# Optimization experiments

Measured on AMD Instinct MI355X. Metric: run time of the kernel, lower is better.

The kernel has to match this reference:

```python
import jax, jax.numpy as jnp
import numpy as np

B = 16384  # batch
D = 1024   # input_size (== hidden_size, required by the original code)
H = 1024   # hidden_size


def setup_inputs() -> dict:
    key = jax.random.key(0)
    ks = jax.random.split(key, 20)
    s = 0.02
    inp = {
        "x": jax.random.normal(ks[0], (B, D), dtype=jnp.float32),
        "h": jax.random.normal(ks[1], (B, H), dtype=jnp.float32),
        "c_prev": jax.random.normal(ks[2], (B, H), dtype=jnp.float32),
    }
    names = ["i_x", "f_x", "c_x", "o_x", "i_h", "f_h", "c_h", "o_h"]
    for n, name in enumerate(names):
        in_dim = D if name.endswith("_x") else H
        inp["W" + name] = jax.random.normal(ks[3 + 2 * n], (H, in_dim), dtype=jnp.float32) * s
        inp["b" + name] = jax.random.normal(ks[4 + 2 * n], (H,), dtype=jnp.float32) * s
    return inp


def reference(x, h, c_prev,
              Wi_x, bi_x, Wf_x, bf_x, Wc_x, bc_x, Wo_x, bo_x,
              Wi_h, bi_h, Wf_h, bf_h, Wc_h, bc_h, Wo_h, bo_h):
    # NOTE: the original module applies NO sigmoid to the gates; i, f, o are raw affine sums.
    i = x @ Wi_x.T + bi_x + h @ Wi_h.T + bi_h
    f = x @ Wf_x.T + bf_x + h @ Wf_h.T + bf_h
    g = jnp.tanh(x @ Wc_x.T + bc_x + h @ Wc_h.T + bc_h)
    o = x @ Wo_x.T + bo_x + h @ Wo_h.T + bo_h
    c_next = g * i + c_prev * f
    h_next = o * jnp.tanh(c_next)
    return (h_next, c_next)
```

## Files before the change

### kernel.cpp

```cpp
#include <hip/hip_runtime.h>
#include <hip/hip_bf16.h>


#define MROWS 16384
#define NCOLS 1024
#define KTOT  2048

typedef __attribute__((ext_vector_type(8))) short bf16x8;
typedef __attribute__((ext_vector_type(4))) float f32x4;
typedef unsigned int u32;
typedef unsigned short u16;

__device__ __forceinline__ u16 f2bf(float f) {
  union { float f; u32 u; } v; v.f = f;
  u32 r = v.u + 0x7fffu + ((v.u >> 16) & 1u);
  return (u16)(r >> 16);
}

__device__ __forceinline__ bf16x8 pack8(float4 lo, float4 hi) {
  bf16x8 v;
  v[0] = (short)f2bf(lo.x); v[1] = (short)f2bf(lo.y);
  v[2] = (short)f2bf(lo.z); v[3] = (short)f2bf(lo.w);
  v[4] = (short)f2bf(hi.x); v[5] = (short)f2bf(hi.y);
  v[6] = (short)f2bf(hi.z); v[7] = (short)f2bf(hi.w);
  return v;
}

__device__ __forceinline__ float tanh_fast(float x) {
  float e = __expf(2.0f * x);
  return 1.0f - 2.0f / (e + 1.0f);
}

typedef __attribute__((address_space(1))) const u32 gas_u32;
typedef __attribute__((address_space(3))) u32 las_u32;

__device__ __forceinline__ void gl_lds16(const void* g, void* l) {
  __builtin_amdgcn_global_load_lds((gas_u32*)g, (las_u32*)l, 16, 0, 0);
}

__global__ void __launch_bounds__(256) convA(const float* __restrict__ x,
                                             const float* __restrict__ h,
                                             u16* __restrict__ A) {
  u32 t = blockIdx.x * 256u + threadIdx.x;
  #pragma unroll
  for (int i = 0; i < 4; ++i) {
    u32 chunk = t + (u32)i * 1048576u;
    u32 row = chunk >> 8;
    u32 cpos = (chunk & 255u) * 8u;
    const float* src = (cpos < 1024u) ? (x + (size_t)row * 1024 + cpos)
                                      : (h + (size_t)row * 1024 + (cpos - 1024u));
    float4 lo = *(const float4*)src;
    float4 hi = *(const float4*)(src + 4);
    *(bf16x8*)(A + (size_t)chunk * 8) = pack8(lo, hi);
  }
}

__global__ void __launch_bounds__(256) convW(const float* __restrict__ wix, const float* __restrict__ wfx,
                                             const float* __restrict__ wcx, const float* __restrict__ wox,
                                             const float* __restrict__ wih, const float* __restrict__ wfh,
                                             const float* __restrict__ wch, const float* __restrict__ woh,
                                             u16* __restrict__ W) {
  u32 t = blockIdx.x * 256u + threadIdx.x;
  const float* WX[4] = {wix, wfx, wcx, wox};
  const float* WH[4] = {wih, wfh, wch, woh};
  #pragma unroll
  for (int g = 0; g < 4; ++g) {
    u32 c3 = t;
    u32 n = c3 >> 8;
    u32 cpos = (c3 & 255u) * 8u;
    const float* src = (cpos < 1024u) ? (WX[g] + (size_t)n * 1024 + cpos)
                                      : (WH[g] + (size_t)n * 1024 + (cpos - 1024u));
    float4 lo = *(const float4*)src;
    float4 hi = *(const float4*)(src + 4);
    *(bf16x8*)(W + (size_t)g * 2097152 + (size_t)c3 * 8) = pack8(lo, hi);
  }
}

template <bool FAST>
__global__ void __launch_bounds__(256, 2) lstm_gemm(
    const u16* __restrict__ Abf, const u16* __restrict__ Wbf,
    const float* __restrict__ x, const float* __restrict__ h,
    const float* __restrict__ wix, const float* __restrict__ wfx,
    const float* __restrict__ wcx, const float* __restrict__ wox,
    const float* __restrict__ wih, const float* __restrict__ wfh,
    const float* __restrict__ wch, const float* __restrict__ woh,
    const float* __restrict__ bix, const float* __restrict__ bfx,
    const float* __restrict__ bcx, const float* __restrict__ box_,
    const float* __restrict__ bih, const float* __restrict__ bfh,
    const float* __restrict__ bch, const float* __restrict__ boh,
    const float* __restrict__ cprev, float* __restrict__ out) {
  __shared__ alignas(16) u16 sA[128 * 64];
  __shared__ alignas(16) u16 sB[4 * 64 * 64];

  const u32 tid = threadIdx.x;
  const u32 lane = tid & 63u;
  const u32 wid = tid >> 6;
  const u32 wr = wid >> 1, wc = wid & 1u;
  const u32 bidx = blockIdx.x;
  const u32 bm = bidx >> 4, bn = bidx & 15u;

  f32x4 acc[4][4][2];
  #pragma unroll
  for (int g = 0; g < 4; ++g)
    #pragma unroll
    for (int m = 0; m < 4; ++m)
      #pragma unroll
      for (int n = 0; n < 2; ++n)
        acc[g][m][n] = (f32x4){0.f, 0.f, 0.f, 0.f};

  const u32 l15 = lane & 15u, l4 = lane >> 4;

  for (int kt = 0; kt < KTOT / 64; ++kt) {
    const u32 k0 = (u32)kt * 64u;
    if (kt) __syncthreads();

    if constexpr (FAST) {
      #pragma unroll
      for (int j = 0; j < 4; ++j) {
        u32 chunk = (wid * 4u + j) * 64u + lane;
        u32 row = chunk >> 3;
        u32 cole = ((chunk & 7u) * 8u) ^ ((row & 7u) << 3);
        const u16* g = Abf + (size_t)(bm * 128u + row) * KTOT + k0 + cole;
        gl_lds16((const void*)g, (void*)(sA + (wid * 4u + j) * 512u));
      }
      #pragma unroll
      for (int j = 0; j < 8; ++j) {
        u32 chunk = (wid * 8u + j) * 64u + lane;
        u32 gate = chunk >> 9;
        u32 c3 = chunk & 511u;
        u32 row = c3 >> 3;
        u32 cole = ((c3 & 7u) * 8u) ^ ((row & 7u) << 3);
        const u16* g = Wbf + (size_t)gate * 2097152 + (size_t)(bn * 64u + row) * KTOT + k0 + cole;
        gl_lds16((const void*)g, (void*)(sB + (wid * 8u + j) * 512u));
      }
    } else {
      #pragma unroll
      for (int c = 0; c < 4; ++c) {
        u32 chunk = tid + (u32)c * 256u;
        u32 row = chunk >> 3;
        u32 cp = (chunk & 7u) * 8u;
        u32 gk = k0 + cp;
        const float* src = (gk < 1024u) ? (x + (size_t)(bm * 128u + row) * 1024 + gk)
                                        : (h + (size_t)(bm * 128u + row) * 1024 + (gk - 1024u));
        float4 lo = *(const float4*)src;
        float4 hi = *(const float4*)(src + 4);
        u32 dst = row * 128u + ((cp * 2u) ^ ((row & 7u) << 4));
        *(bf16x8*)((char*)sA + dst) = pack8(lo, hi);
      }
      #pragma unroll
      for (int g = 0; g < 4; ++g) {
        const float* Wxg = (g == 0) ? wix : (g == 1) ? wfx : (g == 2) ? wcx : wox;
        const float* Whg = (g == 0) ? wih : (g == 1) ? wfh : (g == 2) ? wch : woh;
        #pragma unroll
        for (int cc = 0; cc < 2; ++cc) {
          u32 c3 = tid + (u32)cc * 256u;
          u32 row = c3 >> 3;
          u32 cp = (c3 & 7u) * 8u;
          u32 gk = k0 + cp;
          const float* src = (gk < 1024u) ? (Wxg + (size_t)(bn * 64u + row) * 1024 + gk)
                                          : (Whg + (size_t)(bn * 64u + row) * 1024 + (gk - 1024u));
          float4 lo = *(const float4*)src;
          float4 hi = *(const float4*)(src + 4);
          u32 dst = (u32)g * 8192u + row * 128u + ((cp * 2u) ^ ((row & 7u) << 4));
          *(bf16x8*)((char*)sB + dst) = pack8(lo, hi);
        }
      }
    }
    __syncthreads();

    #pragma unroll
    for (int s = 0; s < 2; ++s) {
      bf16x8 af[4];
      #pragma unroll
      for (int m = 0; m < 4; ++m) {
        u32 mrow = wr * 64u + (u32)m * 16u + l15;
        u32 off = mrow * 128u + (((u32)s * 64u + l4 * 16u) ^ ((mrow & 7u) << 4));
        af[m] = *(const bf16x8*)((const char*)sA + off);
      }
      #pragma unroll
      for (int g = 0; g < 4; ++g) {
        #pragma unroll
        for (int nf = 0; nf < 2; ++nf) {
          u32 nrow = wc * 32u + (u32)nf * 16u + l15;
          u32 off = (u32)g * 8192u + nrow * 128u +
                    (((u32)s * 64u + l4 * 16u) ^ ((nrow & 7u) << 4));
          bf16x8 bfr = *(const bf16x8*)((const char*)sB + off);
          #pragma unroll
          for (int m = 0; m < 4; ++m)
            acc[g][m][nf] = __builtin_amdgcn_mfma_f32_16x16x32_bf16(af[m], bfr, acc[g][m][nf], 0, 0, 0);
        }
      }
    }
  }

  #pragma unroll
  for (int nf = 0; nf < 2; ++nf) {
    u32 col = bn * 64u + wc * 32u + (u32)nf * 16u + l15;
    float bi = bix[col] + bih[col];
    float bff = bfx[col] + bfh[col];
    float bc = bcx[col] + bch[col];
    float bo = box_[col] + boh[col];
    #pragma unroll
    for (int m = 0; m < 4; ++m) {
      u32 row0 = bm * 128u + wr * 64u + (u32)m * 16u + l4 * 4u;
      #pragma unroll
      for (int r = 0; r < 4; ++r) {
        size_t idx = (size_t)(row0 + (u32)r) * 1024 + col;
        float iv = acc[0][m][nf][r] + bi;
        float fv = acc[1][m][nf][r] + bff;
        float gv = tanh_fast(acc[2][m][nf][r] + bc);
        float ov = acc[3][m][nf][r] + bo;
        float cp = cprev[idx];
        float cn = gv * iv + cp * fv;
        out[idx] = ov * tanh_fast(cn);
        out[(size_t)16777216 + idx] = cn;
      }
    }
  }
}

extern "C" void kernel_launch(void* const* d_in, const int* in_sizes, int n_in,
                              void* d_out, int out_size, void* d_ws, size_t ws_size,
                              hipStream_t stream) {
  const float* x = (const float*)d_in[0];
  const float* h = (const float*)d_in[1];
  const float* cprev = (const float*)d_in[2];
  const float* wix = (const float*)d_in[3];  const float* bix = (const float*)d_in[4];
  const float* wfx = (const float*)d_in[5];  const float* bfx = (const float*)d_in[6];
  const float* wcx = (const float*)d_in[7];  const float* bcx = (const float*)d_in[8];
  const float* wox = (const float*)d_in[9];  const float* box_ = (const float*)d_in[10];
  const float* wih = (const float*)d_in[11]; const float* bih = (const float*)d_in[12];
  const float* wfh = (const float*)d_in[13]; const float* bfh = (const float*)d_in[14];
  const float* wch = (const float*)d_in[15]; const float* bch = (const float*)d_in[16];
  const float* woh = (const float*)d_in[17]; const float* boh = (const float*)d_in[18];
  float* out = (float*)d_out;

  const size_t needA = (size_t)MROWS * KTOT * 2;
  const size_t needW = (size_t)4 * NCOLS * KTOT * 2;

  if (ws_size >= needA + needW) {
    u16* Abf = (u16*)d_ws;
    u16* Wbf = (u16*)((char*)d_ws + needA);
    convA<<<dim3(4096), dim3(256), 0, stream>>>(x, h, Abf);
    convW<<<dim3(1024), dim3(256), 0, stream>>>(wix, wfx, wcx, wox, wih, wfh, wch, woh, Wbf);
    lstm_gemm<true><<<dim3(2048), dim3(256), 0, stream>>>(
        Abf, Wbf, nullptr, nullptr,
        nullptr, nullptr, nullptr, nullptr, nullptr, nullptr, nullptr, nullptr,
        bix, bfx, bcx, box_, bih, bfh, bch, boh, cprev, out);
  } else {
    lstm_gemm<false><<<dim3(2048), dim3(256), 0, stream>>>(
        nullptr, nullptr, x, h,
        wix, wfx, wcx, wox, wih, wfh, wch, woh,
        bix, bfx, bcx, box_, bih, bfh, bch, boh, cprev, out);
  }
}
```

Measured before the change: 319.2 us.

## Replace fast-path GEMM with 256x256-tile, 8-wave, double-buffered ping-pong kernel

Introduces a new fast-path kernel that uses 512-thread blocks computing 256-row by 64-column (times 4 gates) output tiles. It double-buffers LDS with async global-to-LDS loads issued one or two k-tiles ahead, and splits each k-step into four MFMA phases separated by barriers, with raised wave priority around the MFMA blocks. Blocks are remapped with a grid swizzle for L2 locality, and the gates are interleaved so each wave holds all four gates for the same columns. The aim is to raise arithmetic intensity and hide load latency. In exchange it adds heavy barrier synchronisation and register pressure, and occupancy may fall to one block per CU.

Result: slower. 342.3 us (+7.2%).

```diff
diff --git a/kernel.cpp b/kernel.cpp
--- a/kernel.cpp
+++ b/kernel.cpp
@@ -76,9 +76,205 @@
   }
 }
 
-template <bool FAST>
-__global__ void __launch_bounds__(256, 2) lstm_gemm(
+#define SBAR() __builtin_amdgcn_sched_barrier(0)
+
+__global__ void __launch_bounds__(512) lstm_gemm8(
     const u16* __restrict__ Abf, const u16* __restrict__ Wbf,
+    const float* __restrict__ bix, const float* __restrict__ bfx,
+    const float* __restrict__ bcx, const float* __restrict__ box_,
+    const float* __restrict__ bih, const float* __restrict__ bfh,
+    const float* __restrict__ bch, const float* __restrict__ boh,
+    const float* __restrict__ cprev, float* __restrict__ out) {
+  __shared__ alignas(16) u16 sA[2 * 16384];
+  __shared__ alignas(16) u16 sB[2 * 16384];
+
+  const u32 tid = threadIdx.x;
+  const u32 lane = tid & 63u, wid = tid >> 6;
+  const u32 wr = wid >> 2, wc = wid & 3u;
+  const u32 l15 = lane & 15u, l4 = lane >> 4;
+
+  const u32 bid = blockIdx.x;
+  const u32 sid = (bid & 7u) * 128u + (bid >> 3);
+  const u32 bm = sid >> 4, bn = sid & 15u;
+
+  const u16* gA[2][2];
+  const u16* gB[2][2];
+  #pragma unroll
+  for (int h = 0; h < 2; ++h)
+    #pragma unroll
+    for (int j = 0; j < 2; ++j) {
+      u32 chunk = (wid * 2u + (u32)j) * 64u + lane;
+      u32 row = chunk >> 3, c = chunk & 7u;
+      u32 col16 = c ^ (row & 7u);
+      gA[h][j] = Abf + (size_t)(bm * 256u + (u32)h * 128u + row) * KTOT + col16 * 8u;
+      u32 fr = (u32)h * 128u + row;
+      u32 fi = fr >> 4;
+      u32 Wrow = (fi & 3u) * 1024u + bn * 64u + (fi >> 2) * 16u + (fr & 15u);
+      gB[h][j] = Wbf + (size_t)Wrow * KTOT + col16 * 8u;
+    }
+
+#define STAGE_A(ktile, dbuf) do { \
+    gl_lds16(gA[0][0] + (ktile) * 64, sA + (dbuf) * 16384u + (wid * 2u + 0u) * 512u); \
+    gl_lds16(gA[0][1] + (ktile) * 64, sA + (dbuf) * 16384u + (wid * 2u + 1u) * 512u); \
+    gl_lds16(gA[1][0] + (ktile) * 64, sA + (dbuf) * 16384u + 8192u + (wid * 2u + 0u) * 512u); \
+    gl_lds16(gA[1][1] + (ktile) * 64, sA + (dbuf) * 16384u + 8192u + (wid * 2u + 1u) * 512u); } while (0)
+#define STAGE_B_H(ktile, dbuf, hh) do { \
+    gl_lds16(gB[hh][0] + (ktile) * 64, sB + (dbuf) * 16384u + (hh) * 8192u + (wid * 2u + 0u) * 512u); \
+    gl_lds16(gB[hh][1] + (ktile) * 64, sB + (dbuf) * 16384u + (hh) * 8192u + (wid * 2u + 1u) * 512u); } while (0)
+
+  const char* cA = (const char*)sA;
+  const char* cB = (const char*)sB;
+  const u32 swzk[2] = { ((0u * 4u + l4) ^ (l15 & 7u)) << 4, ((1u * 4u + l4) ^ (l15 & 7u)) << 4 };
+
+  f32x4 acc[8][4];
+  #pragma unroll
+  for (int mf = 0; mf < 8; ++mf)
+    #pragma unroll
+    for (int gf = 0; gf < 4; ++gf)
+      acc[mf][gf] = (f32x4){0.f, 0.f, 0.f, 0.f};
+
+  STAGE_A(0, 0);
+  STAGE_B_H(0, 0, 0); STAGE_B_H(0, 0, 1);
+  STAGE_A(1, 1);
+  SBAR();
+  asm volatile("s_waitcnt vmcnt(4)" ::: "memory");
+  __builtin_amdgcn_s_barrier();
+  SBAR();
+
+  #pragma unroll 2
+  for (int kt = 0; kt < 32; ++kt) {
+    const u32 d = (u32)kt & 1u, dn = d ^ 1u;
+    const u32 dA = d * 32768u, dB = d * 32768u;
+    bf16x8 a03[4][2], a47[4][2], b01[2][2], b23[2][2];
+
+    #pragma unroll
+    for (int mf = 0; mf < 4; ++mf) {
+      u32 rb = dA + (wr * 128u + (u32)mf * 16u + l15) * 128u;
+      a03[mf][0] = *(const bf16x8*)(cA + rb + swzk[0]);
+      a03[mf][1] = *(const bf16x8*)(cA + rb + swzk[1]);
+    }
+    #pragma unroll
+    for (int gf = 0; gf < 2; ++gf) {
+      u32 rb = dB + (wc * 64u + (u32)gf * 16u + l15) * 128u;
+      b01[gf][0] = *(const bf16x8*)(cB + rb + swzk[0]);
+      b01[gf][1] = *(const bf16x8*)(cB + rb + swzk[1]);
+    }
+    if (kt < 31) STAGE_B_H(kt + 1, dn, 0);
+    SBAR();
+    __builtin_amdgcn_s_barrier();
+    asm volatile("s_waitcnt lgkmcnt(0)" ::: "memory");
+    SBAR();
+    __builtin_amdgcn_s_setprio(1);
+    #pragma unroll
+    for (int ks = 0; ks < 2; ++ks)
+      #pragma unroll
+      for (int gf = 0; gf < 2; ++gf)
+        #pragma unroll
+        for (int mf = 0; mf < 4; ++mf)
+          acc[mf][gf] = __builtin_amdgcn_mfma_f32_16x16x32_bf16(a03[mf][ks], b01[gf][ks], acc[mf][gf], 0, 0, 0);
+    __builtin_amdgcn_s_setprio(0);
+    SBAR();
+    __builtin_amdgcn_s_barrier();
+    SBAR();
+
+    #pragma unroll
+    for (int gf = 0; gf < 2; ++gf) {
+      u32 rb = dB + (wc * 64u + (2u + (u32)gf) * 16u + l15) * 128u;
+      b23[gf][0] = *(const bf16x8*)(cB + rb + swzk[0]);
+      b23[gf][1] = *(const bf16x8*)(cB + rb + swzk[1]);
+    }
+    if (kt < 31) STAGE_B_H(kt + 1, dn, 1);
+    SBAR();
+    __builtin_amdgcn_s_barrier();
+    asm volatile("s_waitcnt lgkmcnt(0)" ::: "memory");
+    SBAR();
+    __builtin_amdgcn_s_setprio(1);
+    #pragma unroll
+    for (int ks = 0; ks < 2; ++ks)
+      #pragma unroll
+      for (int gf = 0; gf < 2; ++gf)
+        #pragma unroll
+        for (int mf = 0; mf < 4; ++mf)
+          acc[mf][2 + gf] = __builtin_amdgcn_mfma_f32_16x16x32_bf16(a03[mf][ks], b23[gf][ks], acc[mf][2 + gf], 0, 0, 0);
+    __builtin_amdgcn_s_setprio(0);
+    SBAR();
+    __builtin_amdgcn_s_barrier();
+    SBAR();
+
+    #pragma unroll
+    for (int mf = 0; mf < 4; ++mf) {
+      u32 rb = dA + (wr * 128u + (4u + (u32)mf) * 16u + l15) * 128u;
+      a47[mf][0] = *(const bf16x8*)(cA + rb + swzk[0]);
+      a47[mf][1] = *(const bf16x8*)(cA + rb + swzk[1]);
+    }
+    SBAR();
+    __builtin_amdgcn_s_barrier();
+    asm volatile("s_waitcnt lgkmcnt(0)" ::: "memory");
+    SBAR();
+    __builtin_amdgcn_s_setprio(1);
+    #pragma unroll
+    for (int ks = 0; ks < 2; ++ks)
+      #pragma unroll
+      for (int gf = 0; gf < 2; ++gf)
+        #pragma unroll
+        for (int mf = 0; mf < 4; ++mf)
+          acc[4 + mf][gf] = __builtin_amdgcn_mfma_f32_16x16x32_bf16(a47[mf][ks], b01[gf][ks], acc[4 + mf][gf], 0, 0, 0);
+    __builtin_amdgcn_s_setprio(0);
+    SBAR();
+    __builtin_amdgcn_s_barrier();
+    SBAR();
+
+    if (kt < 30) {
+      STAGE_A(kt + 2, d);
+      SBAR();
+      asm volatile("s_waitcnt vmcnt(4)" ::: "memory");
+    } else if (kt == 30) {
+      SBAR();
+      asm volatile("s_waitcnt vmcnt(0)" ::: "memory");
+    }
+    SBAR();
+    __builtin_amdgcn_s_barrier();
+    SBAR();
+    __builtin_amdgcn_s_setprio(1);
+    #pragma unroll
+    for (int ks = 0; ks < 2; ++ks)
+      #pragma unroll
+      for (int gf = 0; gf < 2; ++gf)
+        #pragma unroll
+        for (int mf = 0; mf < 4; ++mf)
+          acc[4 + mf][2 + gf] = __builtin_amdgcn_mfma_f32_16x16x32_bf16(a47[mf][ks], b23[gf][ks], acc[4 + mf][2 + gf], 0, 0, 0);
+    __builtin_amdgcn_s_setprio(0);
+    SBAR();
+    __builtin_amdgcn_s_barrier();
+    SBAR();
+  }
+
+  const u32 col = bn * 64u + wc * 16u + l15;
+  const float bi = bix[col] + bih[col];
+  const float bff = bfx[col] + bfh[col];
+  const float bc = bcx[col] + bch[col];
+  const float bo = box_[col] + boh[col];
+  #pragma unroll
+  for (int mf = 0; mf < 8; ++mf) {
+    u32 row0 = bm * 256u + wr * 128u + (u32)mf * 16u + l4 * 4u;
+    #pragma unroll
+    for (int r = 0; r < 4; ++r) {
+      size_t idx = (size_t)(row0 + (u32)r) * 1024 + col;
+      float iv = acc[mf][0][r] + bi;
+      float fv = acc[mf][1][r] + bff;
+      float gv = tanh_fast(acc[mf][2][r] + bc);
+      float ov = acc[mf][3][r] + bo;
+      float cp = cprev[idx];
+      float cn = gv * iv + cp * fv;
+      out[idx] = ov * tanh_fast(cn);
+      out[(size_t)16777216 + idx] = cn;
+    }
+  }
+#undef STAGE_A
+#undef STAGE_B_H
+}
+
+__global__ void __launch_bounds__(256, 2) lstm_gemm_fb(
     const float* __restrict__ x, const float* __restrict__ h,
     const float* __restrict__ wix, const float* __restrict__ wfx,
     const float* __restrict__ wcx, const float* __restrict__ wox,
@@ -91,14 +287,12 @@
     const float* __restrict__ cprev, float* __restrict__ out) {
   __shared__ alignas(16) u16 sA[128 * 64];
   __shared__ alignas(16) u16 sB[4 * 64 * 64];
-
   const u32 tid = threadIdx.x;
   const u32 lane = tid & 63u;
   const u32 wid = tid >> 6;
   const u32 wr = wid >> 1, wc = wid & 1u;
   const u32 bidx = blockIdx.x;
   const u32 bm = bidx >> 4, bn = bidx & 15u;
-
   f32x4 acc[4][4][2];
   #pragma unroll
   for (int g = 0; g < 4; ++g)
@@ -107,67 +301,42 @@
       #pragma unroll
       for (int n = 0; n < 2; ++n)
         acc[g][m][n] = (f32x4){0.f, 0.f, 0.f, 0.f};
-
   const u32 l15 = lane & 15u, l4 = lane >> 4;
-
   for (int kt = 0; kt < KTOT / 64; ++kt) {
     const u32 k0 = (u32)kt * 64u;
     if (kt) __syncthreads();
-
-    if constexpr (FAST) {
-      #pragma unroll
-      for (int j = 0; j < 4; ++j) {
-        u32 chunk = (wid * 4u + j) * 64u + lane;
-        u32 row = chunk >> 3;
-        u32 cole = ((chunk & 7u) * 8u) ^ ((row & 7u) << 3);
-        const u16* g = Abf + (size_t)(bm * 128u + row) * KTOT + k0 + cole;
-        gl_lds16((const void*)g, (void*)(sA + (wid * 4u + j) * 512u));
-      }
-      #pragma unroll
-      for (int j = 0; j < 8; ++j) {
-        u32 chunk = (wid * 8u + j) * 64u + lane;
-        u32 gate = chunk >> 9;
-        u32 c3 = chunk & 511u;
+    #pragma unroll
+    for (int c = 0; c < 4; ++c) {
+      u32 chunk = tid + (u32)c * 256u;
+      u32 row = chunk >> 3;
+      u32 cp = (chunk & 7u) * 8u;
+      u32 gk = k0 + cp;
+      const float* src = (gk < 1024u) ? (x + (size_t)(bm * 128u + row) * 1024 + gk)
+                                      : (h + (size_t)(bm * 128u + row) * 1024 + (gk - 1024u));
+      float4 lo = *(const float4*)src;
+      float4 hi = *(const float4*)(src + 4);
+      u32 dst = row * 128u + ((cp * 2u) ^ ((row & 7u) << 4));
+      *(bf16x8*)((char*)sA + dst) = pack8(lo, hi);
+    }
+    #pragma unroll
+    for (int g = 0; g < 4; ++g) {
+      const float* Wxg = (g == 0) ? wix : (g == 1) ? wfx : (g == 2) ? wcx : wox;
+      const float* Whg = (g == 0) ? wih : (g == 1) ? wfh : (g == 2) ? wch : woh;
+      #pragma unroll
+      for (int cc = 0; cc < 2; ++cc) {
+        u32 c3 = tid + (u32)cc * 256u;
         u32 row = c3 >> 3;
-        u32 cole = ((c3 & 7u) * 8u) ^ ((row & 7u) << 3);
-        const u16* g = Wbf + (size_t)gate * 2097152 + (size_t)(bn * 64u + row) * KTOT + k0 + cole;
-        gl_lds16((const void*)g, (void*)(sB + (wid * 8u + j) * 512u));
-      }
-    } else {
-      #pragma unroll
-      for (int c = 0; c < 4; ++c) {
-        u32 chunk = tid + (u32)c * 256u;
-        u32 row = chunk >> 3;
-        u32 cp = (chunk & 7u) * 8u;
+        u32 cp = (c3 & 7u) * 8u;
         u32 gk = k0 + cp;
-        const float* src = (gk < 1024u) ? (x + (size_t)(bm * 128u + row) * 1024 + gk)
-                                        : (h + (size_t)(bm * 128u + row) * 1024 + (gk - 1024u));
+        const float* src = (gk < 1024u) ? (Wxg + (size_t)(bn * 64u + row) * 1024 + gk)
+                                        : (Whg + (size_t)(bn * 64u + row) * 1024 + (gk - 1024u));
         float4 lo = *(const float4*)src;
         float4 hi = *(const float4*)(src + 4);
-        u32 dst = row * 128u + ((cp * 2u) ^ ((row & 7u) << 4));
-        *(bf16x8*)((char*)sA + dst) = pack8(lo, hi);
+        u32 dst = (u32)g * 8192u + row * 128u + ((cp * 2u) ^ ((row & 7u) << 4));
+        *(bf16x8*)((char*)sB + dst) = pack8(lo, hi);
       }
-      #pragma unroll
-      for (int g = 0; g < 4; ++g) {
-        const float* Wxg = (g == 0) ? wix : (g == 1) ? wfx : (g == 2) ? wcx : wox;
-        const float* Whg = (g == 0) ? wih : (g == 1) ? wfh : (g == 2) ? wch : woh;
-        #pragma unroll
-        for (int cc = 0; cc < 2; ++cc) {
-          u32 c3 = tid + (u32)cc * 256u;
-          u32 row = c3 >> 3;
-          u32 cp = (c3 & 7u) * 8u;
-          u32 gk = k0 + cp;
-          const float* src = (gk < 1024u) ? (Wxg + (size_t)(bn * 64u + row) * 1024 + gk)
-                                          : (Whg + (size_t)(bn * 64u + row) * 1024 + (gk - 1024u));
-          float4 lo = *(const float4*)src;
-          float4 hi = *(const float4*)(src + 4);
-          u32 dst = (u32)g * 8192u + row * 128u + ((cp * 2u) ^ ((row & 7u) << 4));
-          *(bf16x8*)((char*)sB + dst) = pack8(lo, hi);
-        }
-      }
     }
     __syncthreads();
-
     #pragma unroll
     for (int s = 0; s < 2; ++s) {
       bf16x8 af[4];
@@ -192,7 +361,6 @@
       }
     }
   }
-
   #pragma unroll
   for (int nf = 0; nf < 2; ++nf) {
     u32 col = bn * 64u + wc * 32u + (u32)nf * 16u + l15;
@@ -243,14 +411,11 @@
     u16* Wbf = (u16*)((char*)d_ws + needA);
     convA<<<dim3(4096), dim3(256), 0, stream>>>(x, h, Abf);
     convW<<<dim3(1024), dim3(256), 0, stream>>>(wix, wfx, wcx, wox, wih, wfh, wch, woh, Wbf);
-    lstm_gemm<true><<<dim3(2048), dim3(256), 0, stream>>>(
-        Abf, Wbf, nullptr, nullptr,
-        nullptr, nullptr, nullptr, nullptr, nullptr, nullptr, nullptr, nullptr,
+    lstm_gemm8<<<dim3(1024), dim3(512), 0, stream>>>(
+        Abf, Wbf, bix, bfx, bcx, box_, bih, bfh, bch, boh, cprev, out);
+  } else {
+    lstm_gemm_fb<<<dim3(2048), dim3(256), 0, stream>>>(
+        x, h, wix, wfx, wcx, wox, wih, wfh, wch, woh,
         bix, bfx, bcx, box_, bih, bfh, bch, boh, cprev, out);
-  } else {
-    lstm_gemm<false><<<dim3(2048), dim3(256), 0, stream>>>(
-        nullptr, nullptr, x, h,
-        wix, wfx, wcx, wox, wih, wfh, wch, woh,
-        bix, bfx, bcx, box_, bih, bfh, bch, boh, cprev, out);
-  }
-}
+  }
+}
```

## Rewrite fast GEMM path with 256-row tiles, double-buffered LDS, and XCD-aware block mapping

Applied to the files above, without the earlier changes.

Adds a new fused LSTM GEMM kernel with 512 threads and 256x(4x64) tiles that double-buffers LDS so global-to-LDS loads for the next K tile overlap MFMA work on the current one. Block indices are remapped so neighbouring tiles land on the same XCD for L2 reuse, and wave priority is raised around the MFMA section. The goal is to hide load latency, halve synchronisations per tile, and cut redundant A/W traffic. In exchange it uses 128 KB of LDS per block, allowing only one block per CU, and creates heavy register pressure from 32 accumulators per wave.

After: 357.2 us. +11.9%, slower.

```diff
diff --git a/kernel.cpp b/kernel.cpp
--- a/kernel.cpp
+++ b/kernel.cpp
@@ -76,9 +76,127 @@
   }
 }
 
-template <bool FAST>
-__global__ void __launch_bounds__(256, 2) lstm_gemm(
+__global__ void __launch_bounds__(512) lstm_gemm2(
     const u16* __restrict__ Abf, const u16* __restrict__ Wbf,
+    const float* __restrict__ bix, const float* __restrict__ bfx,
+    const float* __restrict__ bcx, const float* __restrict__ box_,
+    const float* __restrict__ bih, const float* __restrict__ bfh,
+    const float* __restrict__ bch, const float* __restrict__ boh,
+    const float* __restrict__ cprev, float* __restrict__ out) {
+  __shared__ alignas(16) u16 sA[2 * 16384];
+  __shared__ alignas(16) u16 sB[2 * 16384];
+
+  const u32 tid = threadIdx.x;
+  const u32 lane = tid & 63u, wid = tid >> 6;
+  const u32 wr = wid >> 1, wc = wid & 1u;
+  const u32 l15 = lane & 15u, l4 = lane >> 4;
+
+  const u32 bid = blockIdx.x;
+  const u32 sid = (bid & 7u) * 128u + (bid >> 3);
+  const u32 bm = sid >> 4, bn = sid & 15u;
+
+  const u16* gAp[4];
+  const u16* gBp[4];
+  #pragma unroll
+  for (int j = 0; j < 4; ++j) {
+    u32 chunk = wid * 256u + (u32)j * 64u + lane;
+    u32 row = chunk >> 3, k8 = chunk & 7u;
+    u32 col16 = k8 ^ (row & 7u);
+    gAp[j] = Abf + (size_t)(bm * 256u + row) * KTOT + col16 * 8u;
+    u32 Wrow = (row >> 6) * 1024u + bn * 64u + (row & 63u);
+    gBp[j] = Wbf + (size_t)Wrow * KTOT + col16 * 8u;
+  }
+
+#define STAGE(ktile, dbuf) do { \
+    _Pragma("unroll") \
+    for (int j = 0; j < 4; ++j) { \
+      u32 dst = (dbuf) * 16384u + (wid * 256u + (u32)j * 64u) * 8u; \
+      gl_lds16(gAp[j] + (u32)(ktile) * 64u, sA + dst); \
+      gl_lds16(gBp[j] + (u32)(ktile) * 64u, sB + dst); \
+    } \
+  } while (0)
+
+  const char* cA = (const char*)sA;
+  const char* cB = (const char*)sB;
+  const u32 kb[2] = { l4 * 16u, 64u + l4 * 16u };
+
+  f32x4 acc[4][4][2];
+  #pragma unroll
+  for (int mf = 0; mf < 4; ++mf)
+    #pragma unroll
+    for (int g = 0; g < 4; ++g)
+      #pragma unroll
+      for (int nf = 0; nf < 2; ++nf)
+        acc[mf][g][nf] = (f32x4){0.f, 0.f, 0.f, 0.f};
+
+  STAGE(0, 0);
+  __syncthreads();
+
+  #pragma unroll 2
+  for (int kt = 0; kt < 32; ++kt) {
+    const u32 d = (u32)kt & 1u, dn = d ^ 1u;
+    const u32 dO = d * 32768u;
+
+    if (kt < 31) STAGE(kt + 1, dn);
+    __builtin_amdgcn_sched_barrier(0);
+
+    bf16x8 af[4][2];
+    #pragma unroll
+    for (int mf = 0; mf < 4; ++mf) {
+      u32 mrow = wr * 64u + (u32)mf * 16u + l15;
+      u32 rb = dO + mrow * 128u;
+      u32 sw = (mrow & 7u) << 4;
+      af[mf][0] = *(const bf16x8*)(cA + rb + (kb[0] ^ sw));
+      af[mf][1] = *(const bf16x8*)(cA + rb + (kb[1] ^ sw));
+    }
+
+    __builtin_amdgcn_s_setprio(1);
+    #pragma unroll
+    for (int s = 0; s < 2; ++s)
+      #pragma unroll
+      for (int g = 0; g < 4; ++g)
+        #pragma unroll
+        for (int nf = 0; nf < 2; ++nf) {
+          u32 brow = (u32)g * 64u + wc * 32u + (u32)nf * 16u + l15;
+          u32 off = dO + brow * 128u + (kb[s] ^ ((brow & 7u) << 4));
+          bf16x8 bfr = *(const bf16x8*)(cB + off);
+          #pragma unroll
+          for (int mf = 0; mf < 4; ++mf)
+            acc[mf][g][nf] = __builtin_amdgcn_mfma_f32_16x16x32_bf16(af[mf][s], bfr, acc[mf][g][nf], 0, 0, 0);
+        }
+    __builtin_amdgcn_s_setprio(0);
+
+    __syncthreads();
+  }
+#undef STAGE
+
+  #pragma unroll
+  for (int nf = 0; nf < 2; ++nf) {
+    u32 col = bn * 64u + wc * 32u + (u32)nf * 16u + l15;
+    float bi = bix[col] + bih[col];
+    float bff = bfx[col] + bfh[col];
+    float bc = bcx[col] + bch[col];
+    float bo = box_[col] + boh[col];
+    #pragma unroll
+    for (int mf = 0; mf < 4; ++mf) {
+      u32 row0 = bm * 256u + wr * 64u + (u32)mf * 16u + l4 * 4u;
+      #pragma unroll
+      for (int r = 0; r < 4; ++r) {
+        size_t idx = (size_t)(row0 + (u32)r) * 1024 + col;
+        float iv = acc[mf][0][nf][r] + bi;
+        float fv = acc[mf][1][nf][r] + bff;
+        float gv = tanh_fast(acc[mf][2][nf][r] + bc);
+        float ov = acc[mf][3][nf][r] + bo;
+        float cp = cprev[idx];
+        float cn = gv * iv + cp * fv;
+        out[idx] = ov * tanh_fast(cn);
+        out[(size_t)16777216 + idx] = cn;
+      }
+    }
+  }
+}
+
+__global__ void __launch_bounds__(256, 2) lstm_gemm_fb(
     const float* __restrict__ x, const float* __restrict__ h,
     const float* __restrict__ wix, const float* __restrict__ wfx,
     const float* __restrict__ wcx, const float* __restrict__ wox,
@@ -91,14 +209,12 @@
     const float* __restrict__ cprev, float* __restrict__ out) {
   __shared__ alignas(16) u16 sA[128 * 64];
   __shared__ alignas(16) u16 sB[4 * 64 * 64];
-
   const u32 tid = threadIdx.x;
   const u32 lane = tid & 63u;
   const u32 wid = tid >> 6;
   const u32 wr = wid >> 1, wc = wid & 1u;
   const u32 bidx = blockIdx.x;
   const u32 bm = bidx >> 4, bn = bidx & 15u;
-
   f32x4 acc[4][4][2];
   #pragma unroll
   for (int g = 0; g < 4; ++g)
@@ -107,67 +223,42 @@
       #pragma unroll
       for (int n = 0; n < 2; ++n)
         acc[g][m][n] = (f32x4){0.f, 0.f, 0.f, 0.f};
-
   const u32 l15 = lane & 15u, l4 = lane >> 4;
-
   for (int kt = 0; kt < KTOT / 64; ++kt) {
     const u32 k0 = (u32)kt * 64u;
     if (kt) __syncthreads();
-
-    if constexpr (FAST) {
-      #pragma unroll
-      for (int j = 0; j < 4; ++j) {
-        u32 chunk = (wid * 4u + j) * 64u + lane;
-        u32 row = chunk >> 3;
-        u32 cole = ((chunk & 7u) * 8u) ^ ((row & 7u) << 3);
-        const u16* g = Abf + (size_t)(bm * 128u + row) * KTOT + k0 + cole;
-        gl_lds16((const void*)g, (void*)(sA + (wid * 4u + j) * 512u));
-      }
-      #pragma unroll
-      for (int j = 0; j < 8; ++j) {
-        u32 chunk = (wid * 8u + j) * 64u + lane;
-        u32 gate = chunk >> 9;
-        u32 c3 = chunk & 511u;
+    #pragma unroll
+    for (int c = 0; c < 4; ++c) {
+      u32 chunk = tid + (u32)c * 256u;
+      u32 row = chunk >> 3;
+      u32 cp = (chunk & 7u) * 8u;
+      u32 gk = k0 + cp;
+      const float* src = (gk < 1024u) ? (x + (size_t)(bm * 128u + row) * 1024 + gk)
+                                      : (h + (size_t)(bm * 128u + row) * 1024 + (gk - 1024u));
+      float4 lo = *(const float4*)src;
+      float4 hi = *(const float4*)(src + 4);
+      u32 dst = row * 128u + ((cp * 2u) ^ ((row & 7u) << 4));
+      *(bf16x8*)((char*)sA + dst) = pack8(lo, hi);
+    }
+    #pragma unroll
+    for (int g = 0; g < 4; ++g) {
+      const float* Wxg = (g == 0) ? wix : (g == 1) ? wfx : (g == 2) ? wcx : wox;
+      const float* Whg = (g == 0) ? wih : (g == 1) ? wfh : (g == 2) ? wch : woh;
+      #pragma unroll
+      for (int cc = 0; cc < 2; ++cc) {
+        u32 c3 = tid + (u32)cc * 256u;
         u32 row = c3 >> 3;
-        u32 cole = ((c3 & 7u) * 8u) ^ ((row & 7u) << 3);
-        const u16* g = Wbf + (size_t)gate * 2097152 + (size_t)(bn * 64u + row) * KTOT + k0 + cole;
-        gl_lds16((const void*)g, (void*)(sB + (wid * 8u + j) * 512u));
-      }
-    } else {
-      #pragma unroll
-      for (int c = 0; c < 4; ++c) {
-        u32 chunk = tid + (u32)c * 256u;
-        u32 row = chunk >> 3;
-        u32 cp = (chunk & 7u) * 8u;
+        u32 cp = (c3 & 7u) * 8u;
         u32 gk = k0 + cp;
-        const float* src = (gk < 1024u) ? (x + (size_t)(bm * 128u + row) * 1024 + gk)
-                                        : (h + (size_t)(bm * 128u + row) * 1024 + (gk - 1024u));
+        const float* src = (gk < 1024u) ? (Wxg + (size_t)(bn * 64u + row) * 1024 + gk)
+                                        : (Whg + (size_t)(bn * 64u + row) * 1024 + (gk - 1024u));
         float4 lo = *(const float4*)src;
         float4 hi = *(const float4*)(src + 4);
-        u32 dst = row * 128u + ((cp * 2u) ^ ((row & 7u) << 4));
-        *(bf16x8*)((char*)sA + dst) = pack8(lo, hi);
-      }
-      #pragma unroll
-      for (int g = 0; g < 4; ++g) {
-        const float* Wxg = (g == 0) ? wix : (g == 1) ? wfx : (g == 2) ? wcx : wox;
-        const float* Whg = (g == 0) ? wih : (g == 1) ? wfh : (g == 2) ? wch : woh;
-        #pragma unroll
-        for (int cc = 0; cc < 2; ++cc) {
-          u32 c3 = tid + (u32)cc * 256u;
-          u32 row = c3 >> 3;
-          u32 cp = (c3 & 7u) * 8u;
-          u32 gk = k0 + cp;
-          const float* src = (gk < 1024u) ? (Wxg + (size_t)(bn * 64u + row) * 1024 + gk)
-                                          : (Whg + (size_t)(bn * 64u + row) * 1024 + (gk - 1024u));
-          float4 lo = *(const float4*)src;
-          float4 hi = *(const float4*)(src + 4);
-          u32 dst = (u32)g * 8192u + row * 128u + ((cp * 2u) ^ ((row & 7u) << 4));
-          *(bf16x8*)((char*)sB + dst) = pack8(lo, hi);
-        }
+        u32 dst = (u32)g * 8192u + row * 128u + ((cp * 2u) ^ ((row & 7u) << 4));
+        *(bf16x8*)((char*)sB + dst) = pack8(lo, hi);
       }
     }
     __syncthreads();
-
     #pragma unroll
     for (int s = 0; s < 2; ++s) {
       bf16x8 af[4];
@@ -192,7 +283,6 @@
       }
     }
   }
-
   #pragma unroll
   for (int nf = 0; nf < 2; ++nf) {
     u32 col = bn * 64u + wc * 32u + (u32)nf * 16u + l15;
@@ -243,14 +333,11 @@
     u16* Wbf = (u16*)((char*)d_ws + needA);
     convA<<<dim3(4096), dim3(256), 0, stream>>>(x, h, Abf);
     convW<<<dim3(1024), dim3(256), 0, stream>>>(wix, wfx, wcx, wox, wih, wfh, wch, woh, Wbf);
-    lstm_gemm<true><<<dim3(2048), dim3(256), 0, stream>>>(
-        Abf, Wbf, nullptr, nullptr,
-        nullptr, nullptr, nullptr, nullptr, nullptr, nullptr, nullptr, nullptr,
+    lstm_gemm2<<<dim3(1024), dim3(512), 0, stream>>>(
+        Abf, Wbf, bix, bfx, bcx, box_, bih, bfh, bch, boh, cprev, out);
+  } else {
+    lstm_gemm_fb<<<dim3(2048), dim3(256), 0, stream>>>(
+        x, h, wix, wfx, wcx, wox, wih, wfh, wch, woh,
         bix, bfx, bcx, box_, bih, bfh, bch, boh, cprev, out);
-  } else {
-    lstm_gemm<false><<<dim3(2048), dim3(256), 0, stream>>>(
-        nullptr, nullptr, x, h,
-        wix, wfx, wcx, wox, wih, wfh, wch, woh,
-        bix, bfx, bcx, box_, bih, bfh, bch, boh, cprev, out);
-  }
-}
+  }
+}
```
